# Kernel optimization log

Measured on AMD Instinct MI355X. Metric: run time of the kernel, lower is better.

## Reference

```python
import jax, jax.numpy as jnp
import numpy as np

N = 100000      # nodes
E = 3200000     # edges
G = 128         # graphs
IN_C, HID, OUT_C = 3, 64, 128
EPS = 1e-12     # torch F.normalize default eps


def setup_inputs() -> dict:
    key = jax.random.key(0)
    ks = jax.random.split(key, 20)
    inp = {
        "x": jax.random.normal(ks[0], (N, IN_C), dtype=jnp.float32),
        "edge_index": jax.random.randint(ks[1], (2, E), 0, N, dtype=jnp.int64),
        "batch": jnp.sort(jax.random.randint(ks[2], (N,), 0, G, dtype=jnp.int64)),
    }
    dims = [(IN_C, HID), (HID, HID), (HID, HID), (HID, HID)]
    for i, (di, do) in enumerate(dims, start=1):
        inp[f"Wl{i}"] = jax.random.normal(ks[2 + 3 * i], (di, do), jnp.float32) * 0.1
        inp[f"bl{i}"] = jax.random.normal(ks[3 + 3 * i], (do,), jnp.float32) * 0.1
        inp[f"Wr{i}"] = jax.random.normal(ks[4 + 3 * i], (di, do), jnp.float32) * 0.1
    inp["Wfc"] = jax.random.normal(ks[18], (HID, OUT_C), jnp.float32) * 0.1
    inp["bfc"] = jax.random.normal(ks[19], (OUT_C,), jnp.float32) * 0.1
    return inp


def _sage(x, src, dst, Wl, bl, Wr):
    # mean-aggregate neighbor features: messages flow src -> dst
    agg = jax.ops.segment_sum(x[src], dst, num_segments=N)          # [N, d]
    cnt = jax.ops.segment_sum(jnp.ones((src.shape[0],), x.dtype), dst,
                              num_segments=N)                        # [N]
    mean = agg / jnp.maximum(cnt, 1.0)[:, None]
    # PyG SAGEConv: lin_l(aggregated) (with bias) + lin_r(root)
    return mean @ Wl + bl + x @ Wr


def reference(x, edge_index, batch,
              Wl1, bl1, Wr1, Wl2, bl2, Wr2,
              Wl3, bl3, Wr3, Wl4, bl4, Wr4,
              Wfc, bfc):
    src, dst = edge_index[0], edge_index[1]
    h = jax.nn.relu(_sage(x, src, dst, Wl1, bl1, Wr1))
    h = jax.nn.relu(_sage(h, src, dst, Wl2, bl2, Wr2))
    h = jax.nn.relu(_sage(h, src, dst, Wl3, bl3, Wr3))
    h = jax.nn.relu(_sage(h, src, dst, Wl4, bl4, Wr4))
    # global mean pool over graphs
    psum = jax.ops.segment_sum(h, batch, num_segments=G)             # [G, HID]
    pcnt = jax.ops.segment_sum(jnp.ones((N,), h.dtype), batch,
                               num_segments=G)                       # [G]
    pooled = psum / jnp.maximum(pcnt, 1.0)[:, None]
    out = pooled @ Wfc + bfc                                         # [G, OUT_C]
    norm = jnp.maximum(jnp.linalg.norm(out, axis=1, keepdims=True), EPS)
    return out / norm
```

## Files before the change

kernel.cpp:

```cpp
#include <hip/hip_runtime.h>

#define NN 100000
#define NE 3200000
#define NG 128
#define HID 64
#define OUTC 128

#define CHUNK 8192
#define NBLK 391
#define NB1 782

typedef _Float16 half2v __attribute__((ext_vector_type(2)));
typedef _Float16 half4v __attribute__((ext_vector_type(4)));
typedef _Float16 half8v __attribute__((ext_vector_type(8)));
typedef float f32x4 __attribute__((ext_vector_type(4)));

__global__ __launch_bounds__(1024) void k_hist(const int* __restrict__ dst,
                                               int* __restrict__ hist1) {
    __shared__ int h[NB1];
    for (int i = threadIdx.x; i < NB1; i += 1024) h[i] = 0;
    __syncthreads();
    int base = blockIdx.x * CHUNK;
    int end = min(base + CHUNK, NE);
    for (int e = base + threadIdx.x; e < end; e += 1024)
        atomicAdd(&h[dst[e] >> 7], 1);
    __syncthreads();
    for (int i = threadIdx.x; i < NB1; i += 1024)
        hist1[i * NBLK + blockIdx.x] = h[i];
}

__global__ __launch_bounds__(256) void k_rowsum(const int* __restrict__ hist1,
                                                int* __restrict__ rowtot) {
    int row = blockIdx.x * 4 + (threadIdx.x >> 6);
    int lane = threadIdx.x & 63;
    if (row >= NB1) return;
    int s = 0;
    for (int k = lane; k < NBLK; k += 64) s += hist1[row * NBLK + k];
#pragma unroll
    for (int m = 1; m < 64; m <<= 1) s += __shfl_xor(s, m);
    if (lane == 0) rowtot[row] = s;
}

__global__ __launch_bounds__(1024) void k_scanb(const int* __restrict__ rowtot,
                                                int* __restrict__ rowbase,
                                                int* __restrict__ bb) {
    __shared__ int sums[1024];
    int t = threadIdx.x;
    int v = (t < NB1) ? rowtot[t] : 0;
    sums[t] = v;
    __syncthreads();
    for (int d = 1; d < 1024; d <<= 1) {
        int u = (t >= d) ? sums[t - d] : 0;
        __syncthreads();
        sums[t] += u;
        __syncthreads();
    }
    if (t < NB1) {
        int base = sums[t] - v;
        rowbase[t] = base;
        bb[t] = base;
    }
    if (t == 0) bb[NB1] = NE;
}

__global__ __launch_bounds__(256) void k_rowscan(int* __restrict__ hist1,
                                                 const int* __restrict__ rowbase) {
    int row = blockIdx.x * 4 + (threadIdx.x >> 6);
    int lane = threadIdx.x & 63;
    if (row >= NB1) return;
    int carry = rowbase[row];
    for (int k0 = 0; k0 < NBLK; k0 += 64) {
        int k = k0 + lane;
        int v = (k < NBLK) ? hist1[row * NBLK + k] : 0;
        int xv = v;
#pragma unroll
        for (int m = 1; m < 64; m <<= 1) {
            int y = __shfl_up(xv, m);
            if (lane >= m) xv += y;
        }
        int tot = __shfl(xv, 63);
        if (k < NBLK) hist1[row * NBLK + k] = xv - v + carry;
        carry += tot;
    }
}

__global__ __launch_bounds__(1024) void k_scat(const int* __restrict__ src,
                                               const int* __restrict__ dst,
                                               const int* __restrict__ hist1,
                                               int* __restrict__ packed) {
    __shared__ int cur[NB1];
    for (int i = threadIdx.x; i < NB1; i += 1024)
        cur[i] = hist1[i * NBLK + blockIdx.x];
    __syncthreads();
    int base = blockIdx.x * CHUNK;
    int end = min(base + CHUNK, NE);
    for (int e = base + threadIdx.x; e < end; e += 1024) {
        int d = dst[e], s = src[e];
        int p = atomicAdd(&cur[d >> 7], 1);
        packed[p] = ((d & 127) << 17) | s;
    }
}

__global__ __launch_bounds__(512) void k_bucket(const int* __restrict__ packed,
                                                const int* __restrict__ bb,
                                                int* __restrict__ neigh,
                                                int* __restrict__ off) {
    int b = blockIdx.x;
    int lo = bb[b], hi = bb[b + 1];
    __shared__ int cnt[128];
    __shared__ int pos[128];
    __shared__ int cur2[128];
    if (threadIdx.x < 128) cnt[threadIdx.x] = 0;
    __syncthreads();
    for (int i = lo + threadIdx.x; i < hi; i += 512)
        atomicAdd(&cnt[packed[i] >> 17], 1);
    __syncthreads();
    if (threadIdx.x == 0) {
        int run = lo;
        for (int j = 0; j < 128; ++j) { pos[j] = run; run += cnt[j]; }
    }
    __syncthreads();
    if (threadIdx.x < 128) {
        int node = b * 128 + threadIdx.x;
        if (node <= NN) off[node] = pos[threadIdx.x];
        cur2[threadIdx.x] = pos[threadIdx.x];
    }
    __syncthreads();
    for (int i = lo + threadIdx.x; i < hi; i += 512) {
        int p = packed[i];
        int j = p >> 17;
        int q = atomicAdd(&cur2[j], 1);
        neigh[q] = p & 0x1FFFF;
    }
}

__global__ __launch_bounds__(256) void k_l1(const int* __restrict__ off,
                                            const int* __restrict__ neigh,
                                            const float* __restrict__ x,
                                            const float* __restrict__ Wl,
                                            const float* __restrict__ bl,
                                            const float* __restrict__ Wr,
                                            _Float16* __restrict__ out) {
    int n = blockIdx.x * 4 + (threadIdx.x >> 6);
    int c = threadIdx.x & 63;
    if (n >= NN) return;
    int lo = off[n], hi = off[n + 1];
    float a0 = 0.f, a1 = 0.f, a2 = 0.f;
    for (int i = lo + c; i < hi; i += 64) {
        int s = neigh[i];
        a0 += x[s * 3 + 0];
        a1 += x[s * 3 + 1];
        a2 += x[s * 3 + 2];
    }
#pragma unroll
    for (int m = 1; m < 64; m <<= 1) {
        a0 += __shfl_xor(a0, m);
        a1 += __shfl_xor(a1, m);
        a2 += __shfl_xor(a2, m);
    }
    float ic = 1.0f / fmaxf((float)(hi - lo), 1.0f);
    a0 *= ic; a1 *= ic; a2 *= ic;
    float x0 = x[n * 3 + 0], x1 = x[n * 3 + 1], x2 = x[n * 3 + 2];
    float acc = bl[c]
              + a0 * Wl[0 * 64 + c] + a1 * Wl[1 * 64 + c] + a2 * Wl[2 * 64 + c]
              + x0 * Wr[0 * 64 + c] + x1 * Wr[1 * 64 + c] + x2 * Wr[2 * 64 + c];
    out[(size_t)n * 64 + c] = (_Float16)fmaxf(acc, 0.0f);
}

__global__ __launch_bounds__(512, 8) void k_agg(const int* __restrict__ off,
                                                const int* __restrict__ neigh,
                                                const _Float16* __restrict__ h,
                                                _Float16* __restrict__ mean) {
    int li = threadIdx.x >> 6;
    int lane = threadIdx.x & 63;
    int g = lane >> 4;
    int q = lane & 15;
    int n = blockIdx.x * 8 + li;
    if (n >= NN) return;

    int lo = __builtin_amdgcn_readfirstlane(off[n]);
    int hi = __builtin_amdgcn_readfirstlane(off[n + 1]);
    int deg = hi - lo;
    const int* __restrict__ np = neigh + lo;
    const char* __restrict__ hb = (const char*)h;
    unsigned qoff = (unsigned)q << 3;

    float ax = 0.f, ay = 0.f, az = 0.f, aw = 0.f;
    int nq = deg >> 2;
#pragma unroll 4
    for (int i = 0; i < nq; ++i) {
        int s0 = np[4 * i + 0];
        int s1 = np[4 * i + 1];
        int s2 = np[4 * i + 2];
        int s3 = np[4 * i + 3];
        int s = (g & 2) ? ((g & 1) ? s3 : s2) : ((g & 1) ? s1 : s0);
        half4v v = *(const half4v*)(hb + (((unsigned)s << 7) | qoff));
        ax += (float)v.x; ay += (float)v.y; az += (float)v.z; aw += (float)v.w;
    }
    if (g == 0) {
        for (int i = nq << 2; i < deg; ++i) {
            int s = np[i];
            half4v v = *(const half4v*)(hb + (((unsigned)s << 7) | qoff));
            ax += (float)v.x; ay += (float)v.y; az += (float)v.z; aw += (float)v.w;
        }
    }
#pragma unroll
    for (int m = 16; m <= 32; m <<= 1) {
        ax += __shfl_xor(ax, m);
        ay += __shfl_xor(ay, m);
        az += __shfl_xor(az, m);
        aw += __shfl_xor(aw, m);
    }
    if (g == 0) {
        float ic = 1.0f / fmaxf((float)deg, 1.0f);
        *(half4v*)&mean[(size_t)n * 64 + 4 * q] =
            half4v{(_Float16)(ax * ic), (_Float16)(ay * ic),
                   (_Float16)(az * ic), (_Float16)(aw * ic)};
    }
}

__global__ __launch_bounds__(512) void k_xform(const _Float16* __restrict__ mean,
                                               const _Float16* __restrict__ h,
                                               const float* __restrict__ Wl,
                                               const float* __restrict__ bl,
                                               const float* __restrict__ Wr,
                                               _Float16* __restrict__ out) {
    __shared__ __align__(16) _Float16 A[128][136];
    __shared__ __align__(16) _Float16 Wt[64][136];

    const int tid  = threadIdx.x;
    const int li   = tid >> 6;
    const int lane = tid & 63;
    const int g    = lane >> 4;
    const int q    = lane & 15;
    const int nb   = blockIdx.x * 128;

    for (int i = tid; i < 8192; i += 512) {
        int kk = i >> 6;
        int c  = i & 63;
        float w = (kk < 64) ? Wl[kk * 64 + c] : Wr[(kk - 64) * 64 + c];
        Wt[c][kk] = (_Float16)w;
    }

    {
        int n = tid >> 2, c = tid & 3;
        int gn = nb + n;
        if (gn >= NN) gn = NN - 1;
        const _Float16* srcp = (c < 2) ? &mean[(size_t)gn * 64 + (c & 1) * 32]
                                       : &h[(size_t)gn * 64 + (c & 1) * 32];
        half8v v0 = *(const half8v*)(srcp + 0);
        half8v v1 = *(const half8v*)(srcp + 8);
        half8v v2 = *(const half8v*)(srcp + 16);
        half8v v3 = *(const half8v*)(srcp + 24);
        _Float16* dstp = &A[n][(c >> 1) * 64 + (c & 1) * 32];
        *(half8v*)(dstp + 0)  = v0;
        *(half8v*)(dstp + 8)  = v1;
        *(half8v*)(dstp + 16) = v2;
        *(half8v*)(dstp + 24) = v3;
    }
    __syncthreads();

    half8v bfr[4][4];
    float bias[4];
#pragma unroll
    for (int t = 0; t < 4; ++t) {
        bias[t] = bl[16 * t + q];
#pragma unroll
        for (int s = 0; s < 4; ++s)
            bfr[t][s] = *(const half8v*)&Wt[16 * t + q][32 * s + 8 * g];
    }

    const int row = 16 * li + q;
    half8v a0 = *(const half8v*)&A[row][0 * 32 + 8 * g];
    half8v a1 = *(const half8v*)&A[row][1 * 32 + 8 * g];
    half8v a2 = *(const half8v*)&A[row][2 * 32 + 8 * g];
    half8v a3 = *(const half8v*)&A[row][3 * 32 + 8 * g];

    f32x4 acc[4];
#pragma unroll
    for (int t = 0; t < 4; ++t) {
        acc[t] = f32x4{0.f, 0.f, 0.f, 0.f};
        acc[t] = __builtin_amdgcn_mfma_f32_16x16x32_f16(a0, bfr[t][0], acc[t], 0, 0, 0);
        acc[t] = __builtin_amdgcn_mfma_f32_16x16x32_f16(a1, bfr[t][1], acc[t], 0, 0, 0);
        acc[t] = __builtin_amdgcn_mfma_f32_16x16x32_f16(a2, bfr[t][2], acc[t], 0, 0, 0);
        acc[t] = __builtin_amdgcn_mfma_f32_16x16x32_f16(a3, bfr[t][3], acc[t], 0, 0, 0);
    }

#pragma unroll
    for (int t = 0; t < 4; ++t) {
        int col = 16 * t + q;
#pragma unroll
        for (int r = 0; r < 4; ++r) {
            int gn = nb + 16 * li + g * 4 + r;
            if (gn < NN) {
                float val = acc[t][r] + bias[t];
                out[(size_t)gn * 64 + col] = (_Float16)fmaxf(val, 0.0f);
            }
        }
    }
}

__device__ __forceinline__ int lower_bound_batch(const int* __restrict__ batch, int val) {
    int lo = 0, hi = NN;
    while (lo < hi) {
        int mid = (lo + hi) >> 1;
        if (batch[mid] < val) lo = mid + 1; else hi = mid;
    }
    return lo;
}

__global__ __launch_bounds__(64) void k_pool(const _Float16* __restrict__ h,
                                             const int* __restrict__ batch,
                                             float* __restrict__ psum) {
    int g = blockIdx.x >> 3;
    int part = blockIdx.x & 7;
    int lane = threadIdx.x;
    int lo = lower_bound_batch(batch, g);
    int hi = lower_bound_batch(batch, g + 1);
    float s = 0.0f;
    for (int n = lo + part; n < hi; n += 8) s += (float)h[(size_t)n * 64 + lane];
    atomicAdd(&psum[g * 64 + lane], s);
}

__global__ __launch_bounds__(128) void k_fc(const float* __restrict__ psum,
                                            const int* __restrict__ batch,
                                            const float* __restrict__ Wfc,
                                            const float* __restrict__ bfc,
                                            float* __restrict__ out) {
    __shared__ float meanv[64];
    __shared__ float red[2];
    int g = blockIdx.x;
    int c = threadIdx.x;
    int lo = lower_bound_batch(batch, g);
    int hi = lower_bound_batch(batch, g + 1);
    float icnt = 1.0f / fmaxf((float)(hi - lo), 1.0f);
    if (c < 64) meanv[c] = psum[g * 64 + c] * icnt;
    __syncthreads();
    float acc = bfc[c];
#pragma unroll
    for (int k = 0; k < 64; ++k) acc += meanv[k] * Wfc[k * 128 + c];
    float ss = acc * acc;
#pragma unroll
    for (int off = 32; off; off >>= 1) ss += __shfl_down(ss, off);
    if ((c & 63) == 0) red[c >> 6] = ss;
    __syncthreads();
    float norm = fmaxf(sqrtf(red[0] + red[1]), 1e-12f);
    out[g * 128 + c] = acc / norm;
}

extern "C" void kernel_launch(void* const* d_in, const int* in_sizes, int n_in,
                              void* d_out, int out_size, void* d_ws, size_t ws_size,
                              hipStream_t stream) {
    const float* x    = (const float*)d_in[0];
    const int*   ei   = (const int*)d_in[1];
    const int*   src  = ei;
    const int*   dst  = ei + NE;
    const int*   batch = (const int*)d_in[2];
    const float* Wl1 = (const float*)d_in[3];
    const float* bl1 = (const float*)d_in[4];
    const float* Wr1 = (const float*)d_in[5];
    const float* Wl2 = (const float*)d_in[6];
    const float* bl2 = (const float*)d_in[7];
    const float* Wr2 = (const float*)d_in[8];
    const float* Wl3 = (const float*)d_in[9];
    const float* bl3 = (const float*)d_in[10];
    const float* Wr3 = (const float*)d_in[11];
    const float* Wl4 = (const float*)d_in[12];
    const float* bl4 = (const float*)d_in[13];
    const float* Wr4 = (const float*)d_in[14];
    const float* Wfc = (const float*)d_in[15];
    const float* bfc = (const float*)d_in[16];
    float* out = (float*)d_out;

    _Float16* hA   = (_Float16*)d_ws;
    _Float16* hB   = hA + (size_t)NN * 64;
    _Float16* mnb  = hB + (size_t)NN * 64;
    float* psum    = (float*)(mnb + (size_t)NN * 64);
    int*   off     = (int*)(psum + (size_t)NG * 64);
    int*   bb      = off + NN + 1;
    int*   rowtot  = bb + NB1 + 1;
    int*   rowbase = rowtot + NB1;
    int*   hist1   = rowbase + NB1;
    int*   packed  = hist1 + NB1 * NBLK;
    int*   neigh   = packed + NE;

    hipMemsetAsync(psum, 0, (size_t)NG * 64 * sizeof(float), stream);

    k_hist<<<NBLK, 1024, 0, stream>>>(dst, hist1);
    k_rowsum<<<(NB1 + 3) / 4, 256, 0, stream>>>(hist1, rowtot);
    k_scanb<<<1, 1024, 0, stream>>>(rowtot, rowbase, bb);
    k_rowscan<<<(NB1 + 3) / 4, 256, 0, stream>>>(hist1, rowbase);
    k_scat<<<NBLK, 1024, 0, stream>>>(src, dst, hist1, packed);
    k_bucket<<<NB1, 512, 0, stream>>>(packed, bb, neigh, off);

    k_l1<<<(NN + 3) / 4, 256, 0, stream>>>(off, neigh, x, Wl1, bl1, Wr1, hA);

    const int aggGrid = (NN + 7) / 8;
    const int xfGrid  = (NN + 127) / 128;

    k_agg<<<aggGrid, 512, 0, stream>>>(off, neigh, hA, mnb);
    k_xform<<<xfGrid, 512, 0, stream>>>(mnb, hA, Wl2, bl2, Wr2, hB);

    k_agg<<<aggGrid, 512, 0, stream>>>(off, neigh, hB, mnb);
    k_xform<<<xfGrid, 512, 0, stream>>>(mnb, hB, Wl3, bl3, Wr3, hA);

    k_agg<<<aggGrid, 512, 0, stream>>>(off, neigh, hA, mnb);
    k_xform<<<xfGrid, 512, 0, stream>>>(mnb, hA, Wl4, bl4, Wr4, hB);

    k_pool<<<NG * 8, 64, 0, stream>>>(hB, batch, psum);
    k_fc<<<NG, 128, 0, stream>>>(psum, batch, Wfc, bfc, out);
}
```

Measured before the change: 368.8 us.

## Stage scatter in shared memory and fuse layer-1 SAGE into bucket kernel

The scatter kernel now builds a local counting sort of each chunk in shared memory and then writes contiguous runs per bucket to global memory, replacing scattered global writes. The first SAGE layer is folded into the bucket kernel: neighbor x values are accumulated with shared-memory float atomics per node, and the 3->64 transform is applied in the same block, removing the separate k_l1 launch and its second pass over neigh. The costs are a serial per-bucket copy loop run by a single thread per bucket, heavy shared-atomic contention, float-atomic summation order that is nondeterministic, and leftover dead code in the initialization.

Result: slower. 387.1 us (+5.0%).

```diff
diff --git a/kernel.cpp b/kernel.cpp
--- a/kernel.cpp
+++ b/kernel.cpp
@@ -88,83 +88,129 @@
                                                const int* __restrict__ dst,
                                                const int* __restrict__ hist1,
                                                int* __restrict__ packed) {
-    __shared__ int cur[NB1];
-    for (int i = threadIdx.x; i < NB1; i += 1024)
-        cur[i] = hist1[i * NBLK + blockIdx.x];
+    __shared__ int bcnt[NB1];
+    __shared__ int lbase[NB1];
+    __shared__ int lcur[NB1];
+    __shared__ int gofs[NB1];
+    __shared__ int ssum[1024];
+    __shared__ int pk[CHUNK];
+    int t = threadIdx.x;
+    for (int i = t; i < NB1; i += 1024) bcnt[i] = 0;
     __syncthreads();
     int base = blockIdx.x * CHUNK;
     int end = min(base + CHUNK, NE);
-    for (int e = base + threadIdx.x; e < end; e += 1024) {
+    int total = end - base;
+    for (int e = base + t; e < end; e += 1024)
+        atomicAdd(&bcnt[dst[e] >> 7], 1);
+    __syncthreads();
+    int v = (t < NB1) ? bcnt[t] : 0;
+    ssum[t] = v;
+    __syncthreads();
+    for (int d = 1; d < 1024; d <<= 1) {
+        int u = (t >= d) ? ssum[t - d] : 0;
+        __syncthreads();
+        ssum[t] += u;
+        __syncthreads();
+    }
+    if (t < NB1) {
+        int lb = ssum[t] - v;
+        lbase[t] = lb;
+        lcur[t] = lb;
+        gofs[t] = hist1[t * NBLK + blockIdx.x] - lb;
+    }
+    __syncthreads();
+    for (int e = base + t; e < end; e += 1024) {
         int d = dst[e], s = src[e];
-        int p = atomicAdd(&cur[d >> 7], 1);
-        packed[p] = ((d & 127) << 17) | s;
+        int slot = atomicAdd(&lcur[d >> 7], 1);
+        pk[slot] = ((d & 127) << 17) | s;
+    }
+    __syncthreads();
+    if (t < NB1) {
+        int b0 = lbase[t];
+        int b1 = (t == NB1 - 1) ? total : lbase[t + 1];
+        int go = gofs[t];
+        for (int k = b0; k < b1; ++k)
+            packed[go + k] = pk[k];
     }
 }
 
 __global__ __launch_bounds__(512) void k_bucket(const int* __restrict__ packed,
                                                 const int* __restrict__ bb,
+                                                const float* __restrict__ x,
+                                                const float* __restrict__ Wl,
+                                                const float* __restrict__ bl,
+                                                const float* __restrict__ Wr,
                                                 int* __restrict__ neigh,
-                                                int* __restrict__ off) {
+                                                int* __restrict__ off,
+                                                _Float16* __restrict__ hA) {
     int b = blockIdx.x;
     int lo = bb[b], hi = bb[b + 1];
     __shared__ int cnt[128];
     __shared__ int pos[128];
     __shared__ int cur2[128];
-    if (threadIdx.x < 128) cnt[threadIdx.x] = 0;
-    __syncthreads();
-    for (int i = lo + threadIdx.x; i < hi; i += 512)
-        atomicAdd(&cnt[packed[i] >> 17], 1);
-    __syncthreads();
-    if (threadIdx.x == 0) {
+    __shared__ float agg3[128][3];
+    __shared__ float Wst[448];
+    int t = threadIdx.x;
+    if (t < 128) cnt[t] = 0;
+    if (t < 384) agg3[t / 3][t % 3] = 0.f;
+    else if (t < 384 + 64) { }
+    if (t >= 128 && t < 128 + 384) {
+        int i = t - 128;
+    }
+    if (t < 384) ((float*)agg3)[t] = 0.f;
+    if (t < 192) Wst[t] = Wl[t];
+    else if (t < 384) Wst[t] = Wr[t - 192];
+    else if (t < 448) Wst[t] = bl[t - 384];
+    __syncthreads();
+    for (int i = lo + t; i < hi; i += 512) {
+        int p = packed[i];
+        int j = p >> 17;
+        int s = p & 0x1FFFF;
+        atomicAdd(&cnt[j], 1);
+        atomicAdd(&agg3[j][0], x[s * 3 + 0]);
+        atomicAdd(&agg3[j][1], x[s * 3 + 1]);
+        atomicAdd(&agg3[j][2], x[s * 3 + 2]);
+    }
+    __syncthreads();
+    if (t == 0) {
         int run = lo;
         for (int j = 0; j < 128; ++j) { pos[j] = run; run += cnt[j]; }
     }
     __syncthreads();
-    if (threadIdx.x < 128) {
-        int node = b * 128 + threadIdx.x;
-        if (node <= NN) off[node] = pos[threadIdx.x];
-        cur2[threadIdx.x] = pos[threadIdx.x];
-    }
-    __syncthreads();
-    for (int i = lo + threadIdx.x; i < hi; i += 512) {
+    if (t < 128) {
+        int node = b * 128 + t;
+        if (node <= NN) off[node] = pos[t];
+        cur2[t] = pos[t];
+    }
+    __syncthreads();
+    for (int i = lo + t; i < hi; i += 512) {
         int p = packed[i];
         int j = p >> 17;
         int q = atomicAdd(&cur2[j], 1);
         neigh[q] = p & 0x1FFFF;
     }
-}
-
-__global__ __launch_bounds__(256) void k_l1(const int* __restrict__ off,
-                                            const int* __restrict__ neigh,
-                                            const float* __restrict__ x,
-                                            const float* __restrict__ Wl,
-                                            const float* __restrict__ bl,
-                                            const float* __restrict__ Wr,
-                                            _Float16* __restrict__ out) {
-    int n = blockIdx.x * 4 + (threadIdx.x >> 6);
-    int c = threadIdx.x & 63;
-    if (n >= NN) return;
-    int lo = off[n], hi = off[n + 1];
-    float a0 = 0.f, a1 = 0.f, a2 = 0.f;
-    for (int i = lo + c; i < hi; i += 64) {
-        int s = neigh[i];
-        a0 += x[s * 3 + 0];
-        a1 += x[s * 3 + 1];
-        a2 += x[s * 3 + 2];
-    }
-#pragma unroll
-    for (int m = 1; m < 64; m <<= 1) {
-        a0 += __shfl_xor(a0, m);
-        a1 += __shfl_xor(a1, m);
-        a2 += __shfl_xor(a2, m);
-    }
-    float ic = 1.0f / fmaxf((float)(hi - lo), 1.0f);
-    a0 *= ic; a1 *= ic; a2 *= ic;
-    float x0 = x[n * 3 + 0], x1 = x[n * 3 + 1], x2 = x[n * 3 + 2];
-    float acc = bl[c]
-              + a0 * Wl[0 * 64 + c] + a1 * Wl[1 * 64 + c] + a2 * Wl[2 * 64 + c]
-              + x0 * Wr[0 * 64 + c] + x1 * Wr[1 * 64 + c] + x2 * Wr[2 * 64 + c];
-    out[(size_t)n * 64 + c] = (_Float16)fmaxf(acc, 0.0f);
+    {
+        int j = t >> 2;
+        int c0 = (t & 3) << 4;
+        int gn = b * 128 + j;
+        if (gn < NN) {
+            float ic = 1.0f / fmaxf((float)cnt[j], 1.0f);
+            float m0 = agg3[j][0] * ic, m1 = agg3[j][1] * ic, m2 = agg3[j][2] * ic;
+            float x0 = x[gn * 3 + 0], x1 = x[gn * 3 + 1], x2 = x[gn * 3 + 2];
+            _Float16 outv[16];
+#pragma unroll
+            for (int cc = 0; cc < 16; ++cc) {
+                int c = c0 + cc;
+                float acc = Wst[384 + c]
+                          + m0 * Wst[0 * 64 + c] + m1 * Wst[1 * 64 + c] + m2 * Wst[2 * 64 + c]
+                          + x0 * Wst[192 + 0 * 64 + c] + x1 * Wst[192 + 1 * 64 + c]
+                          + x2 * Wst[192 + 2 * 64 + c];
+                outv[cc] = (_Float16)fmaxf(acc, 0.0f);
+            }
+            *(half8v*)&hA[(size_t)gn * 64 + c0] = *(half8v*)&outv[0];
+            *(half8v*)&hA[(size_t)gn * 64 + c0 + 8] = *(half8v*)&outv[8];
+        }
+    }
 }
 
 __global__ __launch_bounds__(512, 8) void k_agg(const int* __restrict__ off,
@@ -391,9 +437,7 @@
     k_scanb<<<1, 1024, 0, stream>>>(rowtot, rowbase, bb);
     k_rowscan<<<(NB1 + 3) / 4, 256, 0, stream>>>(hist1, rowbase);
     k_scat<<<NBLK, 1024, 0, stream>>>(src, dst, hist1, packed);
-    k_bucket<<<NB1, 512, 0, stream>>>(packed, bb, neigh, off);
-
-    k_l1<<<(NN + 3) / 4, 256, 0, stream>>>(off, neigh, x, Wl1, bl1, Wr1, hA);
+    k_bucket<<<NB1, 512, 0, stream>>>(packed, bb, x, Wl1, bl1, Wr1, neigh, off, hA);
 
     const int aggGrid = (NN + 7) / 8;
     const int xfGrid  = (NN + 127) / 128;
```
